# Optimization experiments

Measured on AMD Instinct MI355X. Metric: run time of the kernel, lower is better.

Reference implementation:

```python
import jax, jax.numpy as jnp
import numpy as np

N_NODES = 100000
N_EDGES = 3200000
NUM_GRAPHS = 512
D_IN, D_H = 7, 16


def gcn_conv(x, edge_index, W, b, n_nodes):
    # PyG GCNConv: x' = D^{-1/2} (A + I) D^{-1/2} X W + b
    h = x @ W  # [N, d_out] -- do the tiny GEMM first (fewer bytes moved per edge)
    row, col = edge_index[0], edge_index[1]  # messages flow row -> col
    loop = jnp.arange(n_nodes)
    row = jnp.concatenate([row, loop])
    col = jnp.concatenate([col, loop])
    deg = jax.ops.segment_sum(jnp.ones(row.shape[0], dtype=h.dtype), col,
                              num_segments=n_nodes)
    dinv = jnp.where(deg > 0, jax.lax.rsqrt(deg), 0.0)
    norm = dinv[row] * dinv[col]                      # [E+N]
    msg = h[row] * norm[:, None]                      # gather + scale
    out = jax.ops.segment_sum(msg, col, num_segments=n_nodes)  # scatter-add
    return out + b


def setup_inputs() -> dict:
    key = jax.random.key(0)
    ks = jax.random.split(key, 9)
    x = jax.random.normal(ks[0], (N_NODES, D_IN), dtype=jnp.float32)
    edge_index = jax.random.randint(ks[1], (2, N_EDGES), 0, N_NODES, dtype=jnp.int64)
    batch = jnp.sort(jax.random.randint(ks[2], (N_NODES,), 0, NUM_GRAPHS, dtype=jnp.int64))
    def glorot(k, fan_in, fan_out):
        lim = np.sqrt(6.0 / (fan_in + fan_out)).astype(np.float32)
        return jax.random.uniform(k, (fan_in, fan_out), jnp.float32, -lim, lim)
    return {
        "x": x, "edge_index": edge_index, "batch": batch,
        "W1": glorot(ks[3], D_IN, D_H), "b1": jnp.zeros((D_H,), jnp.float32),
        "W2": glorot(ks[4], D_H, D_H), "b2": jnp.zeros((D_H,), jnp.float32),
        "Wl": glorot(ks[5], D_H, 1),   "bl": jnp.zeros((1,), jnp.float32),
    }


def reference(x, edge_index, batch, W1, b1, W2, b2, Wl, bl):
    n = x.shape[0]
    h = jax.nn.relu(gcn_conv(x, edge_index, W1, b1, n))
    h = jax.nn.relu(gcn_conv(h, edge_index, W2, b2, n))
    # global_mean_pool over graphs
    sums = jax.ops.segment_sum(h, batch, num_segments=NUM_GRAPHS)
    cnts = jax.ops.segment_sum(jnp.ones((n,), h.dtype), batch, num_segments=NUM_GRAPHS)
    pooled = sums / jnp.maximum(cnts, 1.0)[:, None]   # [G, 16]
    out = jax.nn.sigmoid(pooled @ Wl + bl)            # [G, 1]
    return out.squeeze(1)                             # [G]
```

## Files before the change

kernel.cpp:

```cpp
#include <hip/hip_runtime.h>
#include <hip/hip_fp16.h>
#include <math.h>

#define N_NODES    100000
#define N_EDGES    3200000
#define NUM_GRAPHS 512
#define D_IN       7
#define D_H        16
#define D_H2       8
#define SHIFT      7
#define BWIDTH     128
#define NB         782
#define CHUNK      8192
#define NCH        391
#define PC         2
#define PB         2
#define TPH        36
#define HST        (8 * TPH)
#define TP1        36
#define HST1       (4 * TP1)

__global__ void hist_kernel(const int* __restrict__ col, int* __restrict__ cnt) {
    __shared__ int lh[NB];
    int tid = threadIdx.x;
    for (int i = tid; i < NB; i += blockDim.x) lh[i] = 0;
    __syncthreads();
    int e0 = blockIdx.x * CHUNK;
    int e1 = e0 + CHUNK; if (e1 > N_EDGES) e1 = N_EDGES;
    for (int e = e0 + tid; e < e1; e += blockDim.x)
        atomicAdd(&lh[col[e] >> SHIFT], 1);
    __syncthreads();
    int* outp = cnt + (size_t)blockIdx.x * NB;
    for (int i = tid; i < NB; i += blockDim.x) outp[i] = lh[i];
}

__global__ void colscan_kernel(const int* __restrict__ cnt, int* __restrict__ base,
                               int* __restrict__ bcnt) {
    __shared__ int ts[256];
    int b = blockIdx.x;
    int tid = threadIdx.x;
    int c0 = tid * PC;
    int vals[PC];
    int sum = 0;
#pragma unroll
    for (int q = 0; q < PC; ++q) {
        int c = c0 + q;
        int v = (c < NCH) ? cnt[(size_t)c * NB + b] : 0;
        vals[q] = v; sum += v;
    }
    ts[tid] = sum;
    __syncthreads();
    for (int st = 1; st < 256; st <<= 1) {
        int v = (tid >= st) ? ts[tid - st] : 0;
        __syncthreads();
        ts[tid] += v;
        __syncthreads();
    }
    int run = ts[tid] - sum;
    int* bp = base + (size_t)b * NCH;
#pragma unroll
    for (int q = 0; q < PC; ++q) {
        int c = c0 + q;
        if (c < NCH) { bp[c] = run; run += vals[q]; }
    }
    if (tid == 0) bcnt[b] = ts[255];
}

__global__ void scan_kernel(const int* __restrict__ bcnt, int* __restrict__ offs) {
    __shared__ int lds[1024];
    int tid = threadIdx.x;
    lds[tid] = (tid < NB) ? bcnt[tid] : 0;
    __syncthreads();
    for (int st = 1; st < 1024; st <<= 1) {
        int v = (tid >= st) ? lds[tid - st] : 0;
        __syncthreads();
        lds[tid] += v;
        __syncthreads();
    }
    if (tid < NB) offs[tid + 1] = lds[tid];
    if (tid == 0) offs[0] = 0;
}

__global__ void place_kernel(const int* __restrict__ row, const int* __restrict__ col,
                             const int* __restrict__ base, const int* __restrict__ offs,
                             int* __restrict__ part) {
    __shared__ int lh[NB];
    __shared__ int sc[NB];
    __shared__ int lb[NB];
    __shared__ int ts[512];
    __shared__ int stage[CHUNK];
    __shared__ int dstv[CHUNK];

    int c = blockIdx.x;
    int tid = threadIdx.x;
    int e0 = c * CHUNK;
    int e1 = e0 + CHUNK; if (e1 > N_EDGES) e1 = N_EDGES;
    int n  = e1 - e0;

    for (int i = tid; i < NB; i += blockDim.x) lh[i] = 0;
    __syncthreads();
    for (int e = e0 + tid; e < e1; e += blockDim.x)
        atomicAdd(&lh[col[e] >> SHIFT], 1);
    __syncthreads();
    int b0 = tid * PB;
    int vals[PB];
    int sum = 0;
#pragma unroll
    for (int q = 0; q < PB; ++q) {
        int b = b0 + q;
        int v = (b < NB) ? lh[b] : 0;
        vals[q] = v; sum += v;
    }
    ts[tid] = sum;
    __syncthreads();
    for (int st = 1; st < 512; st <<= 1) {
        int v = (tid >= st) ? ts[tid - st] : 0;
        __syncthreads();
        ts[tid] += v;
        __syncthreads();
    }
    int run = ts[tid] - sum;
#pragma unroll
    for (int q = 0; q < PB; ++q) {
        int b = b0 + q;
        if (b < NB) {
            sc[b] = run;
            lb[b] = offs[b] + base[(size_t)b * NCH + c];
            run += vals[q];
            lh[b] = 0;
        }
    }
    __syncthreads();
    for (int e = e0 + tid; e < e1; e += blockDim.x) {
        int cc = col[e];
        int b = cc >> SHIFT;
        int rank = atomicAdd(&lh[b], 1);
        int loc = sc[b] + rank;
        stage[loc] = (row[e] << SHIFT) | (cc & (BWIDTH - 1));
        dstv[loc]  = lb[b] + rank;
    }
    __syncthreads();
    for (int i = tid; i < n; i += blockDim.x)
        part[dstv[i]] = stage[i];
}

__global__ void csr_kernel(const int* __restrict__ part, const int* __restrict__ offs,
                           int* __restrict__ csr, int* __restrict__ node_off,
                           int* __restrict__ deg, float* __restrict__ dinv) {
    __shared__ int cnt[BWIDTH];
    __shared__ int scn[BWIDTH];
    __shared__ int cur[BWIDTH];
    int b = blockIdx.x;
    int o0 = offs[b], o1 = offs[b + 1];
    if (threadIdx.x < BWIDTH) cnt[threadIdx.x] = 0;
    __syncthreads();
    for (int j = o0 + threadIdx.x; j < o1; j += blockDim.x)
        atomicAdd(&cnt[part[j] & (BWIDTH - 1)], 1);
    __syncthreads();
    if (threadIdx.x < BWIDTH) scn[threadIdx.x] = cnt[threadIdx.x];
    __syncthreads();
    for (int st = 1; st < BWIDTH; st <<= 1) {
        int v = 0;
        if (threadIdx.x < BWIDTH && threadIdx.x >= st) v = scn[threadIdx.x - st];
        __syncthreads();
        if (threadIdx.x < BWIDTH) scn[threadIdx.x] += v;
        __syncthreads();
    }
    if (threadIdx.x < BWIDTH) {
        int excl = scn[threadIdx.x] - cnt[threadIdx.x];
        cur[threadIdx.x] = excl;
        int c = b * BWIDTH + threadIdx.x;
        if (c < N_NODES) {
            node_off[c] = o0 + excl;
            deg[c] = cnt[threadIdx.x];
            dinv[c] = rsqrtf((float)cnt[threadIdx.x] + 1.0f);
        }
    }
    __syncthreads();
    for (int j = o0 + threadIdx.x; j < o1; j += blockDim.x) {
        int e = part[j];
        int l = e & (BWIDTH - 1);
        int pos = atomicAdd(&cur[l], 1);
        csr[o0 + pos] = e >> SHIFT;
    }
}

__global__ void xs_kernel(const float* __restrict__ x, const float* __restrict__ dinv,
                          unsigned* __restrict__ xsh) {
    int v = blockIdx.x * blockDim.x + threadIdx.x;
    if (v >= N_NODES) return;
    float dv = dinv[v];
    float xv[8];
#pragma unroll
    for (int j = 0; j < D_IN; ++j) xv[j] = x[v * D_IN + j] * dv;
    xv[7] = 0.f;
#pragma unroll
    for (int w = 0; w < 4; ++w) {
        __half2 p = __floats2half2_rn(xv[2 * w], xv[2 * w + 1]);
        xsh[(size_t)v * 4 + w] = *(unsigned*)&p;
    }
}

__global__ void __launch_bounds__(256, 8)
pull1_kernel(const unsigned* __restrict__ xsh, const int* __restrict__ csr,
             const int* __restrict__ node_off, const int* __restrict__ deg,
             const float* __restrict__ dinv, const float* __restrict__ b1,
             const float* __restrict__ W1, const float* __restrict__ W2,
             unsigned* __restrict__ s2h) {
    __shared__ unsigned stage[4][2 * HST1];
    __shared__ float aggrow[4][2][8];
    __shared__ float hrow[4][2][D_H];
    int wave = threadIdx.x >> 6;
    int lane = threadIdx.x & 63;
    int h = lane >> 5, l = lane & 31;
    int v = blockIdx.x * 8 + wave * 2 + h;
    int k = l & 15;
    float w1c[D_IN];
#pragma unroll
    for (int j = 0; j < D_IN; ++j) w1c[j] = W1[j * D_H + k];
    float w2c[D_H];
#pragma unroll
    for (int j = 0; j < D_H; ++j) w2c[j] = W2[j * D_H + k];
    int d = deg[v], o0 = node_off[v];
    unsigned* stg = stage[wave] + h * HST1;
    int rg = l >> 3, p = l & 7;
    int w = p >> 1;
    bool hi = (p & 1);
    const uint4* rp = (const uint4*)(stg + w * TP1 + rg * 8);
    float acc = 0.f;
    for (int base = 0; base < d; base += 32) {
        int j = base + l;
        uint4 a = make_uint4(0u, 0u, 0u, 0u);
        if (j < d) {
            int r = __builtin_nontemporal_load(&csr[o0 + j]);
            a = *(const uint4*)(xsh + (size_t)r * 4);
        }
        asm volatile("s_waitcnt lgkmcnt(0)" ::: "memory");
        stg[0 * TP1 + l] = a.x;
        stg[1 * TP1 + l] = a.y;
        stg[2 * TP1 + l] = a.z;
        stg[3 * TP1 + l] = a.w;
        asm volatile("s_waitcnt lgkmcnt(0)" ::: "memory");
        uint4 q0 = rp[0], q1 = rp[1];
        unsigned ws[8] = { q0.x, q0.y, q0.z, q0.w, q1.x, q1.y, q1.z, q1.w };
#pragma unroll
        for (int i = 0; i < 8; ++i) {
            __half2 ph = *(__half2*)&ws[i];
            acc += hi ? __high2float(ph) : __low2float(ph);
        }
    }
    acc += __shfl_xor(acc, 8, 64);
    acc += __shfl_xor(acc, 16, 64);
    float dv = dinv[v];
    if (l < 8) aggrow[wave][h][l] = acc;
    asm volatile("s_waitcnt lgkmcnt(0)" ::: "memory");
    uint4 sx = *(const uint4*)(xsh + (size_t)v * 4);
    unsigned sxw[4] = { sx.x, sx.y, sx.z, sx.w };
    const float* ag = aggrow[wave][h];
    float hv = b1[k];
#pragma unroll
    for (int j = 0; j < D_IN; ++j) {
        __half2 ph = *(__half2*)&sxw[j >> 1];
        float xsv = (j & 1) ? __high2float(ph) : __low2float(ph);
        hv += dv * (ag[j] + xsv) * w1c[j];
    }
    hv = fmaxf(hv, 0.f);
    if (l < 16) hrow[wave][h][k] = hv;
    asm volatile("s_waitcnt lgkmcnt(0)" ::: "memory");
    const float4* hp = (const float4*)hrow[wave][h];
    float4 h0 = hp[0], h1 = hp[1], h2 = hp[2], h3 = hp[3];
    float a2 = h0.x * w2c[0] + h0.y * w2c[1] + h0.z * w2c[2] + h0.w * w2c[3]
             + h1.x * w2c[4] + h1.y * w2c[5] + h1.z * w2c[6] + h1.w * w2c[7]
             + h2.x * w2c[8] + h2.y * w2c[9] + h2.z * w2c[10] + h2.w * w2c[11]
             + h3.x * w2c[12] + h3.y * w2c[13] + h3.z * w2c[14] + h3.w * w2c[15];
    a2 *= dv;
    float a2hi = __shfl_xor(a2, 1, 64);
    if (l < 16 && (k & 1) == 0) {
        __half2 pq = __floats2half2_rn(a2, a2hi);
        s2h[(size_t)v * D_H2 + (k >> 1)] = *(unsigned*)&pq;
    }
}

__device__ __forceinline__ float gather_half(const unsigned* __restrict__ sh,
                                             const int* __restrict__ csr,
                                             int o0, int d, unsigned* stg, int l) {
    int g = l >> 4, k = l & 15;
    const uint4* rp = (const uint4*)(stg + (k >> 1) * TPH + g * 16);
    bool hi = (k & 1);
    float acc = 0.f;
    for (int base = 0; base < d; base += 32) {
        int j = base + l;
        uint4 a = make_uint4(0u, 0u, 0u, 0u), b = make_uint4(0u, 0u, 0u, 0u);
        if (j < d) {
            int r = __builtin_nontemporal_load(&csr[o0 + j]);
            const uint4* sp = (const uint4*)(sh + (size_t)r * D_H2);
            a = sp[0];
            b = sp[1];
        }
        asm volatile("s_waitcnt lgkmcnt(0)" ::: "memory");
        stg[0 * TPH + l] = a.x;
        stg[1 * TPH + l] = a.y;
        stg[2 * TPH + l] = a.z;
        stg[3 * TPH + l] = a.w;
        stg[4 * TPH + l] = b.x;
        stg[5 * TPH + l] = b.y;
        stg[6 * TPH + l] = b.z;
        stg[7 * TPH + l] = b.w;
        asm volatile("s_waitcnt lgkmcnt(0)" ::: "memory");
        uint4 q0 = rp[0], q1 = rp[1], q2 = rp[2], q3 = rp[3];
        unsigned ws[16] = { q0.x, q0.y, q0.z, q0.w, q1.x, q1.y, q1.z, q1.w,
                            q2.x, q2.y, q2.z, q2.w, q3.x, q3.y, q3.z, q3.w };
#pragma unroll
        for (int i = 0; i < 16; ++i) {
            __half2 p = *(__half2*)&ws[i];
            acc += hi ? __high2float(p) : __low2float(p);
        }
    }
    acc += __shfl_xor(acc, 16, 64);
    return acc;
}

__global__ void __launch_bounds__(256, 8)
pull2_kernel(const unsigned* __restrict__ sh, const int* __restrict__ csr,
             const int* __restrict__ node_off, const int* __restrict__ deg,
             const float* __restrict__ dinv, const float* __restrict__ b2,
             float* __restrict__ h2) {
    __shared__ unsigned stage[4][2 * HST];
    int wave = threadIdx.x >> 6;
    int lane = threadIdx.x & 63;
    int h = lane >> 5, l = lane & 31;
    int v = blockIdx.x * 8 + wave * 2 + h;
    int k = l & 15;
    int d = deg[v], o0 = node_off[v];
    unsigned* stg = stage[wave] + h * HST;
    float acc = gather_half(sh, csr, o0, d, stg, l);
    if (l < 16) {
        float dv = dinv[v];
        unsigned ws = sh[(size_t)v * D_H2 + (k >> 1)];
        __half2 ps = *(__half2*)&ws;
        float selfv = (k & 1) ? __high2float(ps) : __low2float(ps);
        float o = dv * (acc + selfv) + b2[k];
        h2[(size_t)v * D_H + k] = fmaxf(o, 0.f);
    }
}

__global__ void starts_kernel(const int* __restrict__ batch, int* __restrict__ starts) {
    int v = blockIdx.x * blockDim.x + threadIdx.x;
    if (v >= N_NODES) return;
    int bv = batch[v];
    int prev = (v == 0) ? -1 : batch[v - 1];
    for (int g = prev + 1; g <= bv; ++g) starts[g] = v;
    if (v == N_NODES - 1) {
        for (int g = bv + 1; g <= NUM_GRAPHS; ++g) starts[g] = N_NODES;
    }
}

__global__ void pool_head_kernel(const float* __restrict__ h, const int* __restrict__ starts,
                                 const float* __restrict__ Wl, const float* __restrict__ bl,
                                 float* __restrict__ out) {
    int g = blockIdx.x;
    int v0 = starts[g], v1 = starts[g + 1];
    int k = threadIdx.x & 15;
    int vi = threadIdx.x >> 4;
    float acc = 0.f;
    for (int v = v0 + vi; v < v1; v += 16) acc += h[v * D_H + k];
    acc += __shfl_xor(acc, 16, 64);
    acc += __shfl_xor(acc, 32, 64);
    __shared__ float sm[4][D_H];
    int lane = threadIdx.x & 63;
    if (lane < 16) sm[threadIdx.x >> 6][k] = acc;
    __syncthreads();
    if (threadIdx.x < 16) {
        float tot = sm[0][k] + sm[1][k] + sm[2][k] + sm[3][k];
        float cntf = (float)(v1 - v0);
        tot /= fmaxf(cntf, 1.0f);
        float p = tot * Wl[k];
        p += __shfl_xor(p, 1, 64);
        p += __shfl_xor(p, 2, 64);
        p += __shfl_xor(p, 4, 64);
        p += __shfl_xor(p, 8, 64);
        if (k == 0) out[g] = 1.0f / (1.0f + expf(-(p + bl[0])));
    }
}


extern "C" void kernel_launch(void* const* d_in, const int* in_sizes, int n_in,
                              void* d_out, int out_size, void* d_ws, size_t ws_size,
                              hipStream_t stream) {
    const float* x     = (const float*)d_in[0];
    const int*   ei    = (const int*)d_in[1];
    const int*   batch = (const int*)d_in[2];
    const float* W1    = (const float*)d_in[3];
    const float* b1    = (const float*)d_in[4];
    const float* W2    = (const float*)d_in[5];
    const float* b2    = (const float*)d_in[6];
    const float* Wl    = (const float*)d_in[7];
    const float* bl    = (const float*)d_in[8];
    float* out = (float*)d_out;

    const int* row = ei;
    const int* col = ei + N_EDGES;

    char* wsb = (char*)d_ws;
    size_t o = 0;
    int*      part     = (int*)(wsb + o);      o += (size_t)N_EDGES * 4;
    char*     regionA  = wsb + o;              o += (size_t)N_EDGES * 4;
    int*      cnt      = (int*)regionA;
    int*      base     = (int*)(regionA + (size_t)NCH * NB * 4);
    int*      csr      = (int*)regionA;
    int*      bcnt     = (int*)(wsb + o);      o += 1024 * 4;
    int*      offs     = (int*)(wsb + o);      o += 1024 * 4;
    int*      node_off = (int*)(wsb + o);      o += 100352 * 4;
    int*      deg      = (int*)(wsb + o);      o += 100352 * 4;
    float*    dinv     = (float*)(wsb + o);    o += 100352 * 4;
    unsigned* xsh      = (unsigned*)(wsb + o); o += (size_t)N_NODES * 4 * 4;
    unsigned* sBh      = (unsigned*)(wsb + o); o += (size_t)N_NODES * D_H2 * 4;
    float*    h2       = (float*)(wsb + o);    o += (size_t)N_NODES * D_H * 4;
    int*      starts   = (int*)(wsb + o);      o += 1024 * 4;

    const int B = 256;
    const int NVB = (N_NODES + B - 1) / B;

    hist_kernel<<<NCH, 512, 0, stream>>>(col, cnt);
    colscan_kernel<<<NB, B, 0, stream>>>(cnt, base, bcnt);
    scan_kernel<<<1, 1024, 0, stream>>>(bcnt, offs);
    place_kernel<<<NCH, 512, 0, stream>>>(row, col, base, offs, part);
    csr_kernel<<<NB, 512, 0, stream>>>(part, offs, csr, node_off, deg, dinv);

    xs_kernel<<<NVB, B, 0, stream>>>(x, dinv, xsh);
    pull1_kernel<<<N_NODES / 8, B, 0, stream>>>(xsh, csr, node_off, deg, dinv,
                                                b1, W1, W2, sBh);
    pull2_kernel<<<N_NODES / 8, B, 0, stream>>>(sBh, csr, node_off, deg, dinv,
                                                b2, h2);
    starts_kernel<<<NVB, B, 0, stream>>>(batch, starts);
    pool_head_kernel<<<NUM_GRAPHS, B, 0, stream>>>(h2, starts, Wl, bl, out);
}
```

Baseline: 131.8 us.

## Prefetch next neighbor batch in pull kernels and vectorize edge index loads

The gather loops in the layer-1 and layer-2 pull kernels now issue the CSR index and feature loads for the next 32 neighbours before reducing the current batch. This is meant to hide global gather latency behind the LDS transpose and accumulation. The histogram and placement kernels also read col and row as int4 vectors instead of one int per thread. The prefetch raises register pressure, which can lower occupancy under the existing launch bounds.

```diff
diff --git a/kernel.cpp b/kernel.cpp
--- a/kernel.cpp
+++ b/kernel.cpp
@@ -26,9 +26,16 @@
     for (int i = tid; i < NB; i += blockDim.x) lh[i] = 0;
     __syncthreads();
     int e0 = blockIdx.x * CHUNK;
-    int e1 = e0 + CHUNK; if (e1 > N_EDGES) e1 = N_EDGES;
-    for (int e = e0 + tid; e < e1; e += blockDim.x)
-        atomicAdd(&lh[col[e] >> SHIFT], 1);
+    int n  = N_EDGES - e0; if (n > CHUNK) n = CHUNK;
+    int n4 = n >> 2;
+    const int4* cp = (const int4*)(col + e0);
+    for (int q = tid; q < n4; q += blockDim.x) {
+        int4 v = cp[q];
+        atomicAdd(&lh[v.x >> SHIFT], 1);
+        atomicAdd(&lh[v.y >> SHIFT], 1);
+        atomicAdd(&lh[v.z >> SHIFT], 1);
+        atomicAdd(&lh[v.w >> SHIFT], 1);
+    }
     __syncthreads();
     int* outp = cnt + (size_t)blockIdx.x * NB;
     for (int i = tid; i < NB; i += blockDim.x) outp[i] = lh[i];
@@ -94,13 +101,20 @@
     int c = blockIdx.x;
     int tid = threadIdx.x;
     int e0 = c * CHUNK;
-    int e1 = e0 + CHUNK; if (e1 > N_EDGES) e1 = N_EDGES;
-    int n  = e1 - e0;
+    int n  = N_EDGES - e0; if (n > CHUNK) n = CHUNK;
+    int n4 = n >> 2;
+    const int4* cp = (const int4*)(col + e0);
+    const int4* rp = (const int4*)(row + e0);
 
     for (int i = tid; i < NB; i += blockDim.x) lh[i] = 0;
     __syncthreads();
-    for (int e = e0 + tid; e < e1; e += blockDim.x)
-        atomicAdd(&lh[col[e] >> SHIFT], 1);
+    for (int q = tid; q < n4; q += blockDim.x) {
+        int4 v = cp[q];
+        atomicAdd(&lh[v.x >> SHIFT], 1);
+        atomicAdd(&lh[v.y >> SHIFT], 1);
+        atomicAdd(&lh[v.z >> SHIFT], 1);
+        atomicAdd(&lh[v.w >> SHIFT], 1);
+    }
     __syncthreads();
     int b0 = tid * PB;
     int vals[PB];
@@ -131,13 +145,20 @@
         }
     }
     __syncthreads();
-    for (int e = e0 + tid; e < e1; e += blockDim.x) {
-        int cc = col[e];
-        int b = cc >> SHIFT;
-        int rank = atomicAdd(&lh[b], 1);
-        int loc = sc[b] + rank;
-        stage[loc] = (row[e] << SHIFT) | (cc & (BWIDTH - 1));
-        dstv[loc]  = lb[b] + rank;
+    for (int q = tid; q < n4; q += blockDim.x) {
+        int4 cc4 = cp[q];
+        int4 rr4 = rp[q];
+        int ccs[4] = { cc4.x, cc4.y, cc4.z, cc4.w };
+        int rrs[4] = { rr4.x, rr4.y, rr4.z, rr4.w };
+#pragma unroll
+        for (int t = 0; t < 4; ++t) {
+            int cc = ccs[t];
+            int b = cc >> SHIFT;
+            int rank = atomicAdd(&lh[b], 1);
+            int loc = sc[b] + rank;
+            stage[loc] = (rrs[t] << SHIFT) | (cc & (BWIDTH - 1));
+            dstv[loc]  = lb[b] + rank;
+        }
     }
     __syncthreads();
     for (int i = tid; i < n; i += blockDim.x)
@@ -228,12 +249,17 @@
     bool hi = (p & 1);
     const uint4* rp = (const uint4*)(stg + w * TP1 + rg * 8);
     float acc = 0.f;
+    uint4 a = make_uint4(0u, 0u, 0u, 0u);
+    if (l < d) {
+        int r = __builtin_nontemporal_load(&csr[o0 + l]);
+        a = *(const uint4*)(xsh + (size_t)r * 4);
+    }
     for (int base = 0; base < d; base += 32) {
-        int j = base + l;
-        uint4 a = make_uint4(0u, 0u, 0u, 0u);
-        if (j < d) {
-            int r = __builtin_nontemporal_load(&csr[o0 + j]);
-            a = *(const uint4*)(xsh + (size_t)r * 4);
+        uint4 an = make_uint4(0u, 0u, 0u, 0u);
+        int jn = base + 32 + l;
+        if (jn < d) {
+            int r = __builtin_nontemporal_load(&csr[o0 + jn]);
+            an = *(const uint4*)(xsh + (size_t)r * 4);
         }
         asm volatile("s_waitcnt lgkmcnt(0)" ::: "memory");
         stg[0 * TP1 + l] = a.x;
@@ -248,6 +274,7 @@
             __half2 ph = *(__half2*)&ws[i];
             acc += hi ? __high2float(ph) : __low2float(ph);
         }
+        a = an;
     }
     acc += __shfl_xor(acc, 8, 64);
     acc += __shfl_xor(acc, 16, 64);
@@ -281,21 +308,38 @@
     }
 }
 
-__device__ __forceinline__ float gather_half(const unsigned* __restrict__ sh,
-                                             const int* __restrict__ csr,
-                                             int o0, int d, unsigned* stg, int l) {
-    int g = l >> 4, k = l & 15;
+__global__ void __launch_bounds__(256, 8)
+pull2_kernel(const unsigned* __restrict__ sh, const int* __restrict__ csr,
+             const int* __restrict__ node_off, const int* __restrict__ deg,
+             const float* __restrict__ dinv, const float* __restrict__ b2,
+             float* __restrict__ h2) {
+    __shared__ unsigned stage[4][2 * HST];
+    int wave = threadIdx.x >> 6;
+    int lane = threadIdx.x & 63;
+    int h = lane >> 5, l = lane & 31;
+    int v = blockIdx.x * 8 + wave * 2 + h;
+    int k = l & 15;
+    int d = deg[v], o0 = node_off[v];
+    unsigned* stg = stage[wave] + h * HST;
+    int g = l >> 4;
     const uint4* rp = (const uint4*)(stg + (k >> 1) * TPH + g * 16);
     bool hi = (k & 1);
     float acc = 0.f;
+    uint4 a = make_uint4(0u, 0u, 0u, 0u), b = make_uint4(0u, 0u, 0u, 0u);
+    if (l < d) {
+        int r = __builtin_nontemporal_load(&csr[o0 + l]);
+        const uint4* sp = (const uint4*)(sh + (size_t)r * D_H2);
+        a = sp[0];
+        b = sp[1];
+    }
     for (int base = 0; base < d; base += 32) {
-        int j = base + l;
-        uint4 a = make_uint4(0u, 0u, 0u, 0u), b = make_uint4(0u, 0u, 0u, 0u);
-        if (j < d) {
-            int r = __builtin_nontemporal_load(&csr[o0 + j]);
+        uint4 an = make_uint4(0u, 0u, 0u, 0u), bn = make_uint4(0u, 0u, 0u, 0u);
+        int jn = base + 32 + l;
+        if (jn < d) {
+            int r = __builtin_nontemporal_load(&csr[o0 + jn]);
             const uint4* sp = (const uint4*)(sh + (size_t)r * D_H2);
-            a = sp[0];
-            b = sp[1];
+            an = sp[0];
+            bn = sp[1];
         }
         asm volatile("s_waitcnt lgkmcnt(0)" ::: "memory");
         stg[0 * TPH + l] = a.x;
@@ -315,29 +359,13 @@
             __half2 p = *(__half2*)&ws[i];
             acc += hi ? __high2float(p) : __low2float(p);
         }
+        a = an; b = bn;
     }
     acc += __shfl_xor(acc, 16, 64);
-    return acc;
-}
-
-__global__ void __launch_bounds__(256, 8)
-pull2_kernel(const unsigned* __restrict__ sh, const int* __restrict__ csr,
-             const int* __restrict__ node_off, const int* __restrict__ deg,
-             const float* __restrict__ dinv, const float* __restrict__ b2,
-             float* __restrict__ h2) {
-    __shared__ unsigned stage[4][2 * HST];
-    int wave = threadIdx.x >> 6;
-    int lane = threadIdx.x & 63;
-    int h = lane >> 5, l = lane & 31;
-    int v = blockIdx.x * 8 + wave * 2 + h;
-    int k = l & 15;
-    int d = deg[v], o0 = node_off[v];
-    unsigned* stg = stage[wave] + h * HST;
-    float acc = gather_half(sh, csr, o0, d, stg, l);
     if (l < 16) {
         float dv = dinv[v];
-        unsigned ws = sh[(size_t)v * D_H2 + (k >> 1)];
-        __half2 ps = *(__half2*)&ws;
+        unsigned wsv = sh[(size_t)v * D_H2 + (k >> 1)];
+        __half2 ps = *(__half2*)&wsv;
         float selfv = (k & 1) ? __high2float(ps) : __low2float(ps);
         float o = dv * (acc + selfv) + b2[k];
         h2[(size_t)v * D_H + k] = fmaxf(o, 0.f);
```

Measured after the change: 121.4 us. -7.9%, faster.
